# Performance work log

Hardware: AMD Instinct MI355X
Metric: run time of the kernel (lower is better)

The kernel has to match this reference:

```python
import jax, jax.numpy as jnp
import numpy as np

N_EMBD = 1024
N_HEAD = 16
HEAD_DIM = N_EMBD // N_HEAD


def setup_inputs() -> dict:
    key = jax.random.key(0)
    ks = jax.random.split(key, 5)
    B, T, C = 4, 2048, N_EMBD
    x = jax.random.normal(ks[0], (B, T, C), dtype=jnp.float32)
    # torch Linear: y = x @ W.T + b; store W in [out, in] like torch
    scale = 1.0 / np.sqrt(C)
    W_attn = jax.random.normal(ks[1], (3 * C, C), dtype=jnp.float32) * scale
    b_attn = jnp.zeros((3 * C,), dtype=jnp.float32)
    W_proj = jax.random.normal(ks[2], (C, C), dtype=jnp.float32) * scale
    b_proj = jnp.zeros((C,), dtype=jnp.float32)
    return {"x": x, "W_attn": W_attn, "b_attn": b_attn, "W_proj": W_proj, "b_proj": b_proj}


def reference(x, W_attn, b_attn, W_proj, b_proj):
    B, T, C = x.shape
    H, D = N_HEAD, HEAD_DIM
    qkv = x @ W_attn.T + b_attn                    # [B,T,3C]
    q, k, v = jnp.split(qkv, 3, axis=-1)
    q = q.reshape(B, T, H, D).transpose(0, 2, 1, 3)  # [B,H,T,D]
    k = k.reshape(B, T, H, D).transpose(0, 2, 1, 3)
    v = v.reshape(B, T, H, D).transpose(0, 2, 1, 3)
    att = jnp.einsum('bhtd,bhsd->bhts', q, k) / jnp.sqrt(jnp.float32(D))  # [B,H,T,T]
    causal = jnp.tril(jnp.ones((T, T), dtype=bool))
    att = jnp.where(causal[None, None], att, -jnp.inf)
    att = jax.nn.softmax(att, axis=-1)
    # dropout is identity in eval mode (pdrop=0.0)
    y = jnp.einsum('bhts,bhsd->bhtd', att, v)      # [B,H,T,D]
    y = y.transpose(0, 2, 1, 3).reshape(B, T, C)
    return y @ W_proj.T + b_proj
```

## Files before the change

### kernel.cpp

```cpp
#include <hip/hip_runtime.h>
#include <stdint.h>


#define SEQ 2048
#define NBATCH 4
#define CEMB 1024
#define NHEAD 16
#define DHEAD 64
#define BTROWS (NBATCH * SEQ)

typedef __bf16 bf16x8 __attribute__((ext_vector_type(8)));
typedef float f32x4 __attribute__((ext_vector_type(4)));
typedef uint32_t u32x4 __attribute__((ext_vector_type(4)));
typedef unsigned short u16;

__device__ __forceinline__ u16 f2bf(float f) {
  union { float f; uint32_t u; } x; x.f = f;
  uint32_t u = x.u;
  return (u16)((u + 0x7FFFu + ((u >> 16) & 1u)) >> 16);
}

__device__ __forceinline__ void gload_lds16(const void* g, void* l) {
  __builtin_amdgcn_global_load_lds(
      (const __attribute__((address_space(1))) uint32_t*)g,
      (__attribute__((address_space(3))) uint32_t*)l, 16, 0, 0);
}

__global__ __launch_bounds__(256) void cvt_f32_bf16_kernel(
    const float* __restrict__ in, u16* __restrict__ out, int n4) {
  int i = blockIdx.x * blockDim.x + threadIdx.x;
  int stride = gridDim.x * blockDim.x;
  for (; i < n4; i += stride) {
    float4 v = reinterpret_cast<const float4*>(in)[i];
    ushort4 o;
    o.x = f2bf(v.x); o.y = f2bf(v.y); o.z = f2bf(v.z); o.w = f2bf(v.w);
    reinterpret_cast<ushort4*>(out)[i] = o;
  }
}

template <bool OUT_BF16>
__global__ __launch_bounds__(256) void gemm_bt_kernel(
    const u16* __restrict__ A, const u16* __restrict__ Bt,
    const float* __restrict__ bias, void* __restrict__ Cout,
    int M, int N, int K) {
  __shared__ u16 As[128][64];
  __shared__ u16 Bs[128][64];
  const int tid = threadIdx.x;
  const int lane = tid & 63;
  const int wave = tid >> 6;
  const int wr = wave >> 1, wc = wave & 1;
  const int m0 = blockIdx.y * 128;
  const int n0 = blockIdx.x * 128;
  const int l15 = lane & 15, lhi = lane >> 4;

  f32x4 acc[4][4];
#pragma unroll
  for (int i = 0; i < 4; i++)
#pragma unroll
    for (int j = 0; j < 4; j++) acc[i][j] = (f32x4){0.f, 0.f, 0.f, 0.f};

  const int srow = lane >> 3;
  const int scol = (lane & 7) * 8;

  for (int kt = 0; kt < K; kt += 64) {
#pragma unroll
    for (int i = 0; i < 4; i++) {
      int rr = (wave * 4 + i) * 8 + srow;
      gload_lds16(A + (size_t)(m0 + rr) * K + kt + scol, &As[(wave * 4 + i) * 8][0]);
      gload_lds16(Bt + (size_t)(n0 + rr) * K + kt + scol, &Bs[(wave * 4 + i) * 8][0]);
    }
    __syncthreads();
#pragma unroll
    for (int ks = 0; ks < 2; ks++) {
      bf16x8 af[4], bfr[4];
#pragma unroll
      for (int mi = 0; mi < 4; mi++)
        af[mi] = *(const bf16x8*)&As[wr * 64 + mi * 16 + l15][ks * 32 + lhi * 8];
#pragma unroll
      for (int ni = 0; ni < 4; ni++)
        bfr[ni] = *(const bf16x8*)&Bs[wc * 64 + ni * 16 + l15][ks * 32 + lhi * 8];
#pragma unroll
      for (int mi = 0; mi < 4; mi++)
#pragma unroll
        for (int ni = 0; ni < 4; ni++)
          acc[mi][ni] = __builtin_amdgcn_mfma_f32_16x16x32_bf16(
              af[mi], bfr[ni], acc[mi][ni], 0, 0, 0);
    }
    __syncthreads();
  }

#pragma unroll
  for (int mi = 0; mi < 4; mi++) {
#pragma unroll
    for (int ni = 0; ni < 4; ni++) {
      int n = n0 + wc * 64 + ni * 16 + l15;
      float bv = bias[n];
#pragma unroll
      for (int r = 0; r < 4; r++) {
        int m = m0 + wr * 64 + mi * 16 + lhi * 4 + r;
        float v = acc[mi][ni][r] + bv;
        if constexpr (OUT_BF16)
          ((u16*)Cout)[(size_t)m * N + n] = f2bf(v);
        else
          ((float*)Cout)[(size_t)m * N + n] = v;
      }
    }
  }
}

__global__ __launch_bounds__(256) void attn_kernel(
    const u16* __restrict__ qkv, u16* __restrict__ yatt) {
  __shared__ u16 Ks[64][64];
  __shared__ u16 Vt[64][72];
  __shared__ u16 Ps[4][16][72];

  const int tid = threadIdx.x;
  const int lane = tid & 63;
  const int wave = tid >> 6;
  const int qt = (int)gridDim.x - 1 - (int)blockIdx.x;
  const int bh = blockIdx.y;
  const int b = bh >> 4, h = bh & 15;
  const int l15 = lane & 15, lhi = lane >> 4;

  const size_t rs = 3 * CEMB;
  const u16* qb = qkv + (size_t)b * SEQ * rs + h * DHEAD;
  const u16* kb = qb + CEMB;
  const u16* vb = qb + 2 * CEMB;

  const int q0 = qt * 64;

  bf16x8 qf[2];
  {
    const u16* qp = qb + (size_t)(q0 + wave * 16 + l15) * rs + lhi * 8;
    qf[0] = *(const bf16x8*)qp;
    qf[1] = *(const bf16x8*)(qp + 32);
  }

  float m_acc = -1e30f, l_acc = 0.f;
  f32x4 o_acc[4];
#pragma unroll
  for (int dc = 0; dc < 4; dc++) o_acc[dc] = (f32x4){0.f, 0.f, 0.f, 0.f};

  const float L2E = 1.44269504088896f;
  const float SCL = 0.125f;

  for (int s0 = 0; s0 <= q0; s0 += 64) {
#pragma unroll
    for (int i = 0; i < 4; i++) {
      int krow = (wave * 4 + i) * 8 + (lane >> 3);
      int cb = (lane & 7) ^ (krow & 7);
      gload_lds16(kb + (size_t)(s0 + krow) * rs + cb * 8, &Ks[(wave * 4 + i) * 8][0]);
    }
    {
      const u16* gv = vb + (size_t)(s0 + lane) * rs + wave * 16;
      union { u32x4 q[2]; u16 u[16]; } tv;
      tv.q[0] = *(const u32x4*)gv;
      tv.q[1] = *(const u32x4*)(gv + 8);
#pragma unroll
      for (int j = 0; j < 16; j++) Vt[wave * 16 + j][lane] = tv.u[j];
    }
    __syncthreads();

    f32x4 sf[4];
#pragma unroll
    for (int kc = 0; kc < 4; kc++) {
      f32x4 s = (f32x4){0.f, 0.f, 0.f, 0.f};
      int key = kc * 16 + l15;
#pragma unroll
      for (int dc2 = 0; dc2 < 2; dc2++) {
        int cb = (dc2 * 4 + lhi) ^ (key & 7);
        const bf16x8 kf = *(const bf16x8*)((const u16*)&Ks[key][0] + cb * 8);
        s = __builtin_amdgcn_mfma_f32_16x16x32_bf16(kf, qf[dc2], s, 0, 0, 0);
      }
      sf[kc] = s;
    }

    const bool diag = (s0 == q0);
    float cmax = -1e30f;
#pragma unroll
    for (int kc = 0; kc < 4; kc++) {
#pragma unroll
      for (int r = 0; r < 4; r++) {
        float s = sf[kc][r] * SCL;
        if (diag && (kc * 16 + lhi * 4 + r > wave * 16 + l15)) s = -1e30f;
        sf[kc][r] = s;
        cmax = fmaxf(cmax, s);
      }
    }
    cmax = fmaxf(cmax, __shfl_xor(cmax, 16, 64));
    cmax = fmaxf(cmax, __shfl_xor(cmax, 32, 64));
    float mnew = fmaxf(m_acc, cmax);
    float scf = __builtin_amdgcn_exp2f((m_acc - mnew) * L2E);
    m_acc = mnew;

    float ps = 0.f;
#pragma unroll
    for (int kc = 0; kc < 4; kc++) {
      union { u16 h[4]; uint2 v; } pw;
#pragma unroll
      for (int r = 0; r < 4; r++) {
        float p = __builtin_amdgcn_exp2f((sf[kc][r] - mnew) * L2E);
        ps += p;
        pw.h[r] = f2bf(p);
      }
      *(uint2*)&Ps[wave][l15][kc * 16 + lhi * 4] = pw.v;
    }
    ps += __shfl_xor(ps, 16, 64);
    ps += __shfl_xor(ps, 32, 64);
    l_acc = l_acc * scf + ps;

    float scr[4];
#pragma unroll
    for (int r = 0; r < 4; r++) scr[r] = __shfl(scf, lhi * 4 + r, 64);
#pragma unroll
    for (int dc = 0; dc < 4; dc++)
#pragma unroll
      for (int r = 0; r < 4; r++) o_acc[dc][r] *= scr[r];

    bf16x8 pf0 = *(const bf16x8*)&Ps[wave][l15][lhi * 8];
    bf16x8 pf1 = *(const bf16x8*)&Ps[wave][l15][32 + lhi * 8];
#pragma unroll
    for (int dc = 0; dc < 4; dc++) {
      bf16x8 vf0 = *(const bf16x8*)&Vt[dc * 16 + l15][lhi * 8];
      bf16x8 vf1 = *(const bf16x8*)&Vt[dc * 16 + l15][32 + lhi * 8];
      o_acc[dc] = __builtin_amdgcn_mfma_f32_16x16x32_bf16(pf0, vf0, o_acc[dc], 0, 0, 0);
      o_acc[dc] = __builtin_amdgcn_mfma_f32_16x16x32_bf16(pf1, vf1, o_acc[dc], 0, 0, 0);
    }
    __syncthreads();
  }

  float linv[4];
#pragma unroll
  for (int r = 0; r < 4; r++)
    linv[r] = 1.f / __shfl(l_acc, lhi * 4 + r, 64);
#pragma unroll
  for (int dc = 0; dc < 4; dc++) {
#pragma unroll
    for (int r = 0; r < 4; r++) {
      int t = q0 + wave * 16 + lhi * 4 + r;
      float o = o_acc[dc][r] * linv[r];
      yatt[((size_t)(b * SEQ + t)) * CEMB + h * DHEAD + dc * 16 + l15] = f2bf(o);
    }
  }
}

extern "C" void kernel_launch(void* const* d_in, const int* in_sizes, int n_in,
                              void* d_out, int out_size, void* d_ws, size_t ws_size,
                              hipStream_t stream) {
  const float* x      = (const float*)d_in[0];
  const float* W_attn = (const float*)d_in[1];
  const float* b_attn = (const float*)d_in[2];
  const float* W_proj = (const float*)d_in[3];
  const float* b_proj = (const float*)d_in[4];
  float* out = (float*)d_out;

  u16* Xb   = (u16*)d_ws;
  u16* Wab  = Xb  + (size_t)BTROWS * CEMB;
  u16* Wpb  = Wab + (size_t)3 * CEMB * CEMB;
  u16* QKV  = Wpb + (size_t)CEMB * CEMB;
  u16* Yatt = QKV + (size_t)BTROWS * 3 * CEMB;

  cvt_f32_bf16_kernel<<<2048, 256, 0, stream>>>(x, Xb, BTROWS * CEMB / 4);
  cvt_f32_bf16_kernel<<<1024, 256, 0, stream>>>(W_attn, Wab, 3 * CEMB * CEMB / 4);
  cvt_f32_bf16_kernel<<<512, 256, 0, stream>>>(W_proj, Wpb, CEMB * CEMB / 4);

  gemm_bt_kernel<true><<<dim3(3 * CEMB / 128, BTROWS / 128), 256, 0, stream>>>(
      Xb, Wab, b_attn, QKV, BTROWS, 3 * CEMB, CEMB);

  attn_kernel<<<dim3(SEQ / 64, NBATCH * NHEAD), 256, 0, stream>>>(QKV, Yatt);

  gemm_bt_kernel<false><<<dim3(CEMB / 128, BTROWS / 128), 256, 0, stream>>>(
      Yatt, Wpb, b_proj, out, BTROWS, CEMB, CEMB);
}
```

Before: 383.9 us.

## Rewrite attention with 32x32 MFMA, 128-query tiles, register-resident P and lazy rescale

Measured after the change: 339.1 us. 1.13x faster.

```diff
diff --git a/kernel.cpp b/kernel.cpp
--- a/kernel.cpp
+++ b/kernel.cpp
@@ -11,6 +11,7 @@
 
 typedef __bf16 bf16x8 __attribute__((ext_vector_type(8)));
 typedef float f32x4 __attribute__((ext_vector_type(4)));
+typedef float f32x16 __attribute__((ext_vector_type(16)));
 typedef uint32_t u32x4 __attribute__((ext_vector_type(4)));
 typedef unsigned short u16;
 
@@ -18,6 +19,12 @@
   union { float f; uint32_t u; } x; x.f = f;
   uint32_t u = x.u;
   return (u16)((u + 0x7FFFu + ((u >> 16) & 1u)) >> 16);
+}
+
+__device__ __forceinline__ uint32_t pk2(float a, float b) {
+  union { __bf16 h[2]; uint32_t u; } z;
+  z.h[0] = (__bf16)a; z.h[1] = (__bf16)b;
+  return z.u;
 }
 
 __device__ __forceinline__ void gload_lds16(const void* g, void* l) {
@@ -111,45 +118,45 @@
 __global__ __launch_bounds__(256) void attn_kernel(
     const u16* __restrict__ qkv, u16* __restrict__ yatt) {
   __shared__ u16 Ks[64][64];
-  __shared__ u16 Vt[64][72];
-  __shared__ u16 Ps[4][16][72];
+  __shared__ u16 Vt[64][68];
 
   const int tid = threadIdx.x;
   const int lane = tid & 63;
   const int wave = tid >> 6;
-  const int qt = (int)gridDim.x - 1 - (int)blockIdx.x;
+  const int qt = 15 - (int)blockIdx.x;
   const int bh = blockIdx.y;
   const int b = bh >> 4, h = bh & 15;
-  const int l15 = lane & 15, lhi = lane >> 4;
+  const int l31 = lane & 31, hi = lane >> 5;
 
   const size_t rs = 3 * CEMB;
   const u16* qb = qkv + (size_t)b * SEQ * rs + h * DHEAD;
   const u16* kb = qb + CEMB;
   const u16* vb = qb + 2 * CEMB;
 
-  const int q0 = qt * 64;
-
-  bf16x8 qf[2];
+  const int q0 = qt * 128;
+  const int qabs = q0 + wave * 32 + l31;
+
+  bf16x8 qf[4];
   {
-    const u16* qp = qb + (size_t)(q0 + wave * 16 + l15) * rs + lhi * 8;
-    qf[0] = *(const bf16x8*)qp;
-    qf[1] = *(const bf16x8*)(qp + 32);
+    const u16* qp = qb + (size_t)qabs * rs + hi * 8;
+#pragma unroll
+    for (int dc = 0; dc < 4; dc++) qf[dc] = *(const bf16x8*)(qp + dc * 16);
   }
 
   float m_acc = -1e30f, l_acc = 0.f;
-  f32x4 o_acc[4];
-#pragma unroll
-  for (int dc = 0; dc < 4; dc++) o_acc[dc] = (f32x4){0.f, 0.f, 0.f, 0.f};
-
-  const float L2E = 1.44269504088896f;
-  const float SCL = 0.125f;
-
-  for (int s0 = 0; s0 <= q0; s0 += 64) {
-#pragma unroll
-    for (int i = 0; i < 4; i++) {
-      int krow = (wave * 4 + i) * 8 + (lane >> 3);
-      int cb = (lane & 7) ^ (krow & 7);
-      gload_lds16(kb + (size_t)(s0 + krow) * rs + cb * 8, &Ks[(wave * 4 + i) * 8][0]);
+  f32x16 o_acc[2];
+  o_acc[0] = (f32x16)(0.f);
+  o_acc[1] = (f32x16)(0.f);
+
+  const float SCLL2E = 0.125f * 1.44269504088896f;
+
+  for (int s0 = 0; s0 <= q0 + 64; s0 += 64) {
+#pragma unroll
+    for (int c = 0; c < 2; c++) {
+      int row0 = (c * 4 + wave) * 8;
+      int row = row0 + (lane >> 3);
+      int cb = (lane & 7) ^ (row & 7);
+      gload_lds16(kb + (size_t)(s0 + row) * rs + cb * 8, &Ks[row0][0]);
     }
     {
       const u16* gv = vb + (size_t)(s0 + lane) * rs + wave * 16;
@@ -161,86 +168,113 @@
     }
     __syncthreads();
 
-    f32x4 sf[4];
-#pragma unroll
-    for (int kc = 0; kc < 4; kc++) {
-      f32x4 s = (f32x4){0.f, 0.f, 0.f, 0.f};
-      int key = kc * 16 + l15;
-#pragma unroll
-      for (int dc2 = 0; dc2 < 2; dc2++) {
-        int cb = (dc2 * 4 + lhi) ^ (key & 7);
-        const bf16x8 kf = *(const bf16x8*)((const u16*)&Ks[key][0] + cb * 8);
-        s = __builtin_amdgcn_mfma_f32_16x16x32_bf16(kf, qf[dc2], s, 0, 0, 0);
-      }
-      sf[kc] = s;
-    }
-
-    const bool diag = (s0 == q0);
-    float cmax = -1e30f;
-#pragma unroll
-    for (int kc = 0; kc < 4; kc++) {
-#pragma unroll
-      for (int r = 0; r < 4; r++) {
-        float s = sf[kc][r] * SCL;
-        if (diag && (kc * 16 + lhi * 4 + r > wave * 16 + l15)) s = -1e30f;
-        sf[kc][r] = s;
-        cmax = fmaxf(cmax, s);
-      }
-    }
-    cmax = fmaxf(cmax, __shfl_xor(cmax, 16, 64));
-    cmax = fmaxf(cmax, __shfl_xor(cmax, 32, 64));
-    float mnew = fmaxf(m_acc, cmax);
-    float scf = __builtin_amdgcn_exp2f((m_acc - mnew) * L2E);
-    m_acc = mnew;
-
-    float ps = 0.f;
-#pragma unroll
-    for (int kc = 0; kc < 4; kc++) {
-      union { u16 h[4]; uint2 v; } pw;
-#pragma unroll
-      for (int r = 0; r < 4; r++) {
-        float p = __builtin_amdgcn_exp2f((sf[kc][r] - mnew) * L2E);
-        ps += p;
-        pw.h[r] = f2bf(p);
-      }
-      *(uint2*)&Ps[wave][l15][kc * 16 + lhi * 4] = pw.v;
-    }
-    ps += __shfl_xor(ps, 16, 64);
-    ps += __shfl_xor(ps, 32, 64);
-    l_acc = l_acc * scf + ps;
-
-    float scr[4];
-#pragma unroll
-    for (int r = 0; r < 4; r++) scr[r] = __shfl(scf, lhi * 4 + r, 64);
-#pragma unroll
-    for (int dc = 0; dc < 4; dc++)
-#pragma unroll
-      for (int r = 0; r < 4; r++) o_acc[dc][r] *= scr[r];
-
-    bf16x8 pf0 = *(const bf16x8*)&Ps[wave][l15][lhi * 8];
-    bf16x8 pf1 = *(const bf16x8*)&Ps[wave][l15][32 + lhi * 8];
-#pragma unroll
-    for (int dc = 0; dc < 4; dc++) {
-      bf16x8 vf0 = *(const bf16x8*)&Vt[dc * 16 + l15][lhi * 8];
-      bf16x8 vf1 = *(const bf16x8*)&Vt[dc * 16 + l15][32 + lhi * 8];
-      o_acc[dc] = __builtin_amdgcn_mfma_f32_16x16x32_bf16(pf0, vf0, o_acc[dc], 0, 0, 0);
-      o_acc[dc] = __builtin_amdgcn_mfma_f32_16x16x32_bf16(pf1, vf1, o_acc[dc], 0, 0, 0);
+    const bool active = (s0 <= q0 + wave * 32 + 31);
+    if (active) {
+      f32x16 sf[2];
+#pragma unroll
+      for (int kt = 0; kt < 2; kt++) {
+        f32x16 s = (f32x16)(0.f);
+        int key = kt * 32 + l31;
+#pragma unroll
+        for (int dc = 0; dc < 4; dc++) {
+          int cb = (dc * 2 + hi) ^ (key & 7);
+          const bf16x8 kf = *(const bf16x8*)((const u16*)&Ks[key][0] + cb * 8);
+          s = __builtin_amdgcn_mfma_f32_32x32x16_bf16(kf, qf[dc], s, 0, 0, 0);
+        }
+        sf[kt] = s;
+      }
+
+      if (s0 + 63 > q0 + wave * 32) {
+#pragma unroll
+        for (int kt = 0; kt < 2; kt++)
+#pragma unroll
+          for (int r = 0; r < 16; r++) {
+            int key = s0 + kt * 32 + (r & 3) + 8 * (r >> 2) + 4 * hi;
+            if (key > qabs) sf[kt][r] = -3e38f;
+          }
+      }
+
+      float cmax = sf[0][0];
+#pragma unroll
+      for (int r = 1; r < 16; r++) cmax = fmaxf(cmax, sf[0][r]);
+#pragma unroll
+      for (int r = 0; r < 16; r++) cmax = fmaxf(cmax, sf[1][r]);
+      cmax = fmaxf(cmax, __shfl_xor(cmax, 32, 64));
+
+      if (!__all(cmax <= m_acc + 64.0f)) {
+        float mnew = fmaxf(m_acc, cmax);
+        float scf = __builtin_amdgcn_exp2f((m_acc - mnew) * SCLL2E);
+        m_acc = mnew;
+        l_acc *= scf;
+        float scr[16];
+#pragma unroll
+        for (int r = 0; r < 16; r++)
+          scr[r] = __shfl(scf, (r & 3) + 8 * (r >> 2) + 4 * hi, 64);
+#pragma unroll
+        for (int r = 0; r < 16; r++) {
+          o_acc[0][r] *= scr[r];
+          o_acc[1][r] *= scr[r];
+        }
+      }
+
+      const float c1 = -m_acc * SCLL2E;
+      float ps = 0.f;
+#pragma unroll
+      for (int kt = 0; kt < 2; kt++)
+#pragma unroll
+        for (int r = 0; r < 16; r++) {
+          float p = __builtin_amdgcn_exp2f(fmaf(sf[kt][r], SCLL2E, c1));
+          sf[kt][r] = p;
+          ps += p;
+        }
+      ps += __shfl_xor(ps, 32, 64);
+      l_acc += ps;
+
+      bf16x8 pa[4];
+#pragma unroll
+      for (int ks = 0; ks < 4; ks++) {
+        const int t = ks >> 1;
+        const int ra = (ks & 1) * 8;
+        uint32_t a  = pk2(sf[t][ra + 0], sf[t][ra + 1]);
+        uint32_t b2 = pk2(sf[t][ra + 2], sf[t][ra + 3]);
+        uint32_t cc = pk2(sf[t][ra + 4], sf[t][ra + 5]);
+        uint32_t dd = pk2(sf[t][ra + 6], sf[t][ra + 7]);
+        uint32_t snd0 = hi ? a : cc;
+        uint32_t snd1 = hi ? b2 : dd;
+        uint32_t r0 = __shfl_xor(snd0, 32, 64);
+        uint32_t r1 = __shfl_xor(snd1, 32, 64);
+        union { bf16x8 v; uint32_t w[4]; } u;
+        u.w[0] = hi ? r0 : a;
+        u.w[1] = hi ? r1 : b2;
+        u.w[2] = hi ? cc : r0;
+        u.w[3] = hi ? dd : r1;
+        pa[ks] = u.v;
+      }
+
+#pragma unroll
+      for (int dt = 0; dt < 2; dt++) {
+        const u16* vrow = &Vt[dt * 32 + l31][hi * 8];
+#pragma unroll
+        for (int ks = 0; ks < 4; ks++) {
+          union { bf16x8 v; uint2 d[2]; } u;
+          u.d[0] = *(const uint2*)(vrow + ks * 16);
+          u.d[1] = *(const uint2*)(vrow + ks * 16 + 4);
+          o_acc[dt] = __builtin_amdgcn_mfma_f32_32x32x16_bf16(pa[ks], u.v, o_acc[dt], 0, 0, 0);
+        }
+      }
     }
     __syncthreads();
   }
 
-  float linv[4];
-#pragma unroll
-  for (int r = 0; r < 4; r++)
-    linv[r] = 1.f / __shfl(l_acc, lhi * 4 + r, 64);
-#pragma unroll
-  for (int dc = 0; dc < 4; dc++) {
-#pragma unroll
-    for (int r = 0; r < 4; r++) {
-      int t = q0 + wave * 16 + lhi * 4 + r;
-      float o = o_acc[dc][r] * linv[r];
-      yatt[((size_t)(b * SEQ + t)) * CEMB + h * DHEAD + dc * 16 + l15] = f2bf(o);
-    }
+  float rl = 1.0f / l_acc;
+#pragma unroll
+  for (int r = 0; r < 16; r++) {
+    int crow = (r & 3) + 8 * (r >> 2) + 4 * hi;
+    float linv = __shfl(rl, crow, 64);
+    int t = q0 + wave * 32 + crow;
+    u16* yp = yatt + ((size_t)(b * SEQ + t)) * CEMB + h * DHEAD + l31;
+    yp[0]  = f2bf(o_acc[0][r] * linv);
+    yp[32] = f2bf(o_acc[1][r] * linv);
   }
 }
 
@@ -267,7 +301,7 @@
   gemm_bt_kernel<true><<<dim3(3 * CEMB / 128, BTROWS / 128), 256, 0, stream>>>(
       Xb, Wab, b_attn, QKV, BTROWS, 3 * CEMB, CEMB);
 
-  attn_kernel<<<dim3(SEQ / 64, NBATCH * NHEAD), 256, 0, stream>>>(QKV, Yatt);
+  attn_kernel<<<dim3(SEQ / 128, NBATCH * NHEAD), 256, 0, stream>>>(QKV, Yatt);
 
   gemm_bt_kernel<false><<<dim3(CEMB / 128, BTROWS / 128), 256, 0, stream>>>(
       Yatt, Wpb, b_proj, out, BTROWS, CEMB, CEMB);
```
